# Performance work log

Measured on AMD Instinct MI355X. Metric: run time of the kernel, lower is better.

The kernel has to match this reference:

```python
import jax, jax.numpy as jnp
import numpy as np

NHEAD = 8
ATT_EPS = 1e-6
LN_EPS = 1e-5


def _layernorm(x, g, b):
    mu = jnp.mean(x, axis=-1, keepdims=True)
    var = jnp.mean(jnp.square(x - mu), axis=-1, keepdims=True)
    return (x - mu) * jax.lax.rsqrt(var + LN_EPS) * g + b


def setup_inputs() -> dict:
    key = jax.random.key(0)
    ks = jax.random.split(key, 7)
    N, L, C = 4, 16384, 256
    s = 1.0 / np.sqrt(C)
    return {
        "x": jax.random.normal(ks[0], (N, L, C), jnp.float32),
        "Wq": jax.random.normal(ks[1], (C, C), jnp.float32) * s,
        "Wk": jax.random.normal(ks[2], (C, C), jnp.float32) * s,
        "Wv": jax.random.normal(ks[3], (C, C), jnp.float32) * s,
        "Wm": jax.random.normal(ks[4], (C, C), jnp.float32) * s,
        "W1": jax.random.normal(ks[5], (2 * C, 2 * C), jnp.float32) * (1.0 / np.sqrt(2 * C)),
        "W2": jax.random.normal(ks[6], (2 * C, C), jnp.float32) * (1.0 / np.sqrt(2 * C)),
        "g1": jnp.ones((C,), jnp.float32),
        "b1": jnp.zeros((C,), jnp.float32),
        "g2": jnp.ones((C,), jnp.float32),
        "b2": jnp.zeros((C,), jnp.float32),
    }


def reference(x, Wq, Wk, Wv, Wm, W1, W2, g1, b1, g2, b2):
    N, L, C = x.shape
    H = NHEAD
    D = C // H
    # projections -> [N, L, H, D]
    q = (x @ Wq).reshape(N, L, H, D)
    k = (x @ Wk).reshape(N, L, H, D)
    v = (x @ Wv).reshape(N, L, H, D)
    # elu+1 feature map (linear attention)
    Q = jax.nn.elu(q) + 1.0
    K = jax.nn.elu(k) + 1.0
    v = v / L  # values / v_length
    # KV: [N, H, D, Dv]
    KV = jnp.einsum('nshd,nshv->nhdv', K, v)
    # normalizer Z: [N, L, H]
    Z = 1.0 / (jnp.einsum('nlhd,nhd->nlh', Q, K.sum(axis=1)) + ATT_EPS)
    # queried values, rescaled by v_length
    msg = jnp.einsum('nlhd,nhdv,nlh->nlhv', Q, KV, Z) * L  # [N, L, H, Dv]
    # merge heads + norm1
    msg = msg.reshape(N, L, C) @ Wm
    msg = _layernorm(msg, g1, b1)
    # MLP on concat([x, msg]) + norm2
    h = jnp.concatenate([x, msg], axis=-1) @ W1
    h = jax.nn.relu(h) @ W2
    msg = _layernorm(h, g2, b2)
    return x + msg
```

## Files before the change

kernel.cpp:

```cpp
#include <hip/hip_runtime.h>
#include <hip/hip_bf16.h>
#include <math.h>

#define L_SEQ   16384
#define C_DIM   256
#define N_BATCH 4
#define N_HEAD  8
#define D_H     32
#define M_ROWS  (N_BATCH * L_SEQ)
#define KV_SPLIT 64
#define SLAB_E  ((size_t)M_ROWS * C_DIM)

typedef unsigned short u16;
typedef unsigned int   u32;
typedef short s16x8 __attribute__((ext_vector_type(8)));
typedef float f32x4 __attribute__((ext_vector_type(4)));

__device__ __forceinline__ float bf2f(u32 lo16) { return __uint_as_float(lo16 << 16); }
__device__ __forceinline__ u16 f2bf(float f) {
    u32 u = __float_as_uint(f);
    u32 rb = ((u >> 16) & 1u) + 0x7fffu;
    return (u16)((u + rb) >> 16);
}

__device__ __forceinline__ void gl_lds16(const u16* g, u16* l) {
    __builtin_amdgcn_global_load_lds(
        (__attribute__((address_space(1))) void*)g,
        (__attribute__((address_space(3))) void*)l, 16, 0, 0);
}

__global__ __launch_bounds__(256)
void prep_all(const float* __restrict__ x, u16* __restrict__ xb, int n8,
              const float* __restrict__ Wq, const float* __restrict__ Wk,
              const float* __restrict__ Wv, const float* __restrict__ Wm,
              const float* __restrict__ W1, const float* __restrict__ W2,
              u16* __restrict__ wqkvt, u16* __restrict__ wmt,
              u16* __restrict__ w1t, u16* __restrict__ w2t)
{
    __shared__ float tile[32][33];
    int bt = blockIdx.x;
    if (bt < 2048) {
        int i = bt * 256 + threadIdx.x;
        int stride = 2048 * 256;
        for (; i < n8; i += stride) {
            float4 f0 = ((const float4*)x)[(size_t)i * 2];
            float4 f1 = ((const float4*)x)[(size_t)i * 2 + 1];
            uint4 o;
            o.x = (u32)f2bf(f0.x) | ((u32)f2bf(f0.y) << 16);
            o.y = (u32)f2bf(f0.z) | ((u32)f2bf(f0.w) << 16);
            o.z = (u32)f2bf(f1.x) | ((u32)f2bf(f1.y) << 16);
            o.w = (u32)f2bf(f1.z) | ((u32)f2bf(f1.w) << 16);
            ((uint4*)xb)[i] = o;
        }
        return;
    }
    bt -= 2048;
    const float* src; u16* dst; int K, N, rowoff, tt;
    if (bt < 192)      { int w = bt >> 6; tt = bt & 63;
                         src = (w == 0) ? Wq : (w == 1) ? Wk : Wv;
                         dst = wqkvt; K = 256; N = 256; rowoff = w * 256; }
    else if (bt < 256) { tt = bt - 192; src = Wm; dst = wmt; K = 256; N = 256; rowoff = 0; }
    else if (bt < 512) { tt = bt - 256; src = W1; dst = w1t; K = 512; N = 512; rowoff = 0; }
    else               { tt = bt - 512; src = W2; dst = w2t; K = 512; N = 256; rowoff = 0; }
    int ntx = N >> 5;
    int n0 = (tt % ntx) * 32, k0 = (tt / ntx) * 32;
    int tx = threadIdx.x & 31, ty = threadIdx.x >> 5;
    #pragma unroll
    for (int i = 0; i < 32; i += 8)
        tile[ty + i][tx] = src[(size_t)(k0 + ty + i) * N + n0 + tx];
    __syncthreads();
    #pragma unroll
    for (int i = 0; i < 32; i += 8)
        dst[(size_t)(rowoff + n0 + ty + i) * K + k0 + tx] = f2bf(tile[tx][ty + i]);
}

template<int EPI>
__global__ __launch_bounds__(256)
void gemm128(const u16* __restrict__ A1, const u16* __restrict__ A2,
             int KA, int sA1, int sA2,
             const u16* __restrict__ Bt, int ldb, int bstride,
             u16* __restrict__ C, int ldc, int K, float escale, int nx)
{
    __shared__ __align__(16) u16 smem[16384];

    const int tid = threadIdx.x;
    const int nwg = gridDim.x;
    const int cpx = nwg >> 3;
    const int hb  = blockIdx.x;
    const int lb  = (hb & 7) * cpx + (hb >> 3);
    const int m0 = (lb / nx) * 128;
    const int n0 = (lb % nx) * 128;
    const int w = tid >> 6, lane = tid & 63;
    const int wr = w >> 1, wc = w & 1;
    const int g = lane >> 4, r = lane & 15;

    Bt += (size_t)(m0 / L_SEQ) * bstride;

    const u16 *pA1[2], *pA2[2], *pB[2];
    int loff[2];
    #pragma unroll
    for (int i = 0; i < 2; ++i) {
        int li  = i * 256 + tid;
        int row = li >> 2, kc = li & 3;
        int kcg = kc ^ ((row >> 1) & 3);
        pA1[i] = A1 + (size_t)(m0 + row) * sA1 + kcg * 8;
        pA2[i] = A2 + (size_t)(m0 + row) * sA2 + kcg * 8 - KA;
        pB[i]  = Bt + (size_t)(n0 + row) * ldb + kcg * 8;
        loff[i] = li * 8;
    }

    f32x4 acc[4][4] = {};

    auto stage = [&](int kt, int buf) {
        u16* As_ = smem + buf * 4096;
        u16* Bs_ = smem + 8192 + buf * 4096;
        const int ko = kt * 32;
        #pragma unroll
        for (int i = 0; i < 2; ++i) {
            const u16* Ap = ((ko < KA) ? pA1[i] : pA2[i]) + ko;
            gl_lds16(Ap, &As_[loff[i]]);
            gl_lds16(pB[i] + ko, &Bs_[loff[i]]);
        }
    };

    const int kts = K / 32;
    const int gsw = g ^ ((r >> 1) & 3);
    stage(0, 0);
    for (int kt = 0; kt < kts; ++kt) {
        const int cur = kt & 1;
        asm volatile("s_barrier" ::: "memory");
        if (kt + 1 < kts) {
            stage(kt + 1, cur ^ 1);
            asm volatile("s_waitcnt vmcnt(4)" ::: "memory");
        } else {
            asm volatile("s_waitcnt vmcnt(0)" ::: "memory");
        }
        asm volatile("s_barrier" ::: "memory");

        const u16* Ar = smem + cur * 4096;
        const u16* Br = smem + 8192 + cur * 4096;
        s16x8 a[4], b[4];
        #pragma unroll
        for (int mi = 0; mi < 4; ++mi)
            a[mi] = *(const s16x8*)&Ar[(wr * 64 + mi * 16 + r) * 32 + gsw * 8];
        #pragma unroll
        for (int ni = 0; ni < 4; ++ni)
            b[ni] = *(const s16x8*)&Br[(wc * 64 + ni * 16 + r) * 32 + gsw * 8];
        __builtin_amdgcn_s_setprio(1);
        #pragma unroll
        for (int mi = 0; mi < 4; ++mi)
            #pragma unroll
            for (int ni = 0; ni < 4; ++ni)
                asm volatile("v_mfma_f32_16x16x32_bf16 %0, %1, %2, %0"
                             : "+v"(acc[mi][ni]) : "v"(b[ni]), "v"(a[mi]));
        __builtin_amdgcn_s_setprio(0);
    }

    asm volatile("s_nop 7");
    asm volatile("s_nop 7");

    __syncthreads();
    char* ct = (char*)smem;
    #pragma unroll
    for (int mi = 0; mi < 4; ++mi) {
        int rl = wr * 64 + mi * 16 + r;
        #pragma unroll
        for (int ni = 0; ni < 4; ++ni) {
            int cl = wc * 64 + ni * 16 + g * 4;
            int gc = n0 + cl;
            ushort4 o;
            #pragma unroll
            for (int j = 0; j < 4; ++j) {
                float v = acc[mi][ni][j];
                if (EPI == 3)      v = (v > 0.f) ? v : 0.f;
                else if (EPI == 4) v = (gc < 512) ? ((v > 0.f) ? (v + 1.f) : __expf(v))
                                                  : v * escale;
                (&o.x)[j] = f2bf(v);
            }
            int byte = (rl * 256 + cl * 2) ^ ((rl & 7) << 4);
            *(ushort4*)(ct + byte) = o;
        }
    }
    __syncthreads();
    {
        const int rr = tid >> 4, ck = tid & 15;
        u16* slab = C; int coff = n0;
        if (EPI == 4) {
            slab = (n0 < 256) ? C : (n0 < 512) ? C + SLAB_E : C + 2 * SLAB_E;
            coff = n0 & 255;
        }
        #pragma unroll
        for (int it = 0; it < 8; ++it) {
            int rl = it * 16 + rr;
            int byte = (rl * 256 + ck * 16) ^ ((rl & 7) << 4);
            uint4 val = *(const uint4*)(ct + byte);
            size_t row = (size_t)(m0 + rl);
            if (EPI == 4)
                *(uint4*)(slab + row * 256 + coff + ck * 8) = val;
            else
                *(uint4*)(C + row * (size_t)ldc + coff + ck * 8) = val;
        }
    }
}

template<int EPI>
__global__ __launch_bounds__(256)
void gemm_ln(const u16* __restrict__ A1, const u16* __restrict__ A2,
             int KA, int sA1, int sA2,
             const u16* __restrict__ Bt, int ldb, int bstride,
             u16* __restrict__ C, int ldc, int K, float escale, int nx,
             const float* __restrict__ gw, const float* __restrict__ bw,
             const float* __restrict__ xres, float* __restrict__ outf)
{
    __shared__ __align__(16) u16 smem[24576];
    __shared__ float red[4][2][128];

    const int tid = threadIdx.x;
    const int nwg = gridDim.x;
    const int cpx = nwg >> 3;
    const int hb  = blockIdx.x;
    const int lb  = (hb & 7) * cpx + (hb >> 3);
    const int m0 = (lb / nx) * 128;
    const int n0 = (lb % nx) * 256;
    const int wc = tid >> 6;
    const int lane = tid & 63;
    const int g = lane >> 4, r = lane & 15;

    const u16* Btb = Bt + (size_t)(m0 / L_SEQ) * bstride;

    const u16 *pA1[2], *pA2[2], *pB[4];
    int loffA[2], loffB[4];
    #pragma unroll
    for (int i = 0; i < 2; ++i) {
        int li  = i * 256 + tid;
        int row = li >> 2, kc = li & 3;
        int kcg = kc ^ ((row >> 1) & 3);
        pA1[i] = A1 + (size_t)(m0 + row) * sA1 + kcg * 8;
        pA2[i] = A2 + (size_t)(m0 + row) * sA2 + kcg * 8 - KA;
        loffA[i] = li * 8;
    }
    #pragma unroll
    for (int i = 0; i < 4; ++i) {
        int li  = i * 256 + tid;
        int row = li >> 2, kc = li & 3;
        int kcg = kc ^ ((row >> 1) & 3);
        pB[i] = Btb + (size_t)(n0 + row) * ldb + kcg * 8;
        loffB[i] = li * 8;
    }

    f32x4 acc[8][4] = {};

    auto stage = [&](int kt, int buf) {
        u16* As_ = smem + buf * 4096;
        u16* Bs_ = smem + 8192 + buf * 8192;
        const int ko = kt * 32;
        #pragma unroll
        for (int i = 0; i < 2; ++i) {
            const u16* Ap = ((ko < KA) ? pA1[i] : pA2[i]) + ko;
            gl_lds16(Ap, &As_[loffA[i]]);
        }
        #pragma unroll
        for (int i = 0; i < 4; ++i)
            gl_lds16(pB[i] + ko, &Bs_[loffB[i]]);
    };

    const int kts = K / 32;
    const int gsw = g ^ ((r >> 1) & 3);
    stage(0, 0);
    for (int kt = 0; kt < kts; ++kt) {
        const int cur = kt & 1;
        asm volatile("s_barrier" ::: "memory");
        if (kt + 1 < kts) {
            stage(kt + 1, cur ^ 1);
            asm volatile("s_waitcnt vmcnt(6)" ::: "memory");
        } else {
            asm volatile("s_waitcnt vmcnt(0)" ::: "memory");
        }
        asm volatile("s_barrier" ::: "memory");

        const u16* Ar = smem + cur * 4096;
        const u16* Br = smem + 8192 + cur * 8192;
        s16x8 b[4];
        #pragma unroll
        for (int ni = 0; ni < 4; ++ni)
            b[ni] = *(const s16x8*)&Br[(wc * 64 + ni * 16 + r) * 32 + gsw * 8];
        __builtin_amdgcn_s_setprio(1);
        #pragma unroll
        for (int mi = 0; mi < 8; ++mi) {
            s16x8 av = *(const s16x8*)&Ar[(mi * 16 + r) * 32 + gsw * 8];
            #pragma unroll
            for (int ni = 0; ni < 4; ++ni)
                asm volatile("v_mfma_f32_16x16x32_bf16 %0, %1, %2, %0"
                             : "+v"(acc[mi][ni]) : "v"(b[ni]), "v"(av));
        }
        __builtin_amdgcn_s_setprio(0);
    }

    asm volatile("s_nop 7");
    asm volatile("s_nop 7");

    #pragma unroll
    for (int mi = 0; mi < 8; ++mi) {
        float s = 0.f, s2 = 0.f;
        #pragma unroll
        for (int ni = 0; ni < 4; ++ni)
            #pragma unroll
            for (int j = 0; j < 4; ++j) {
                float v = acc[mi][ni][j];
                s += v; s2 += v * v;
            }
        s  += __shfl_xor(s, 16);  s  += __shfl_xor(s, 32);
        s2 += __shfl_xor(s2, 16); s2 += __shfl_xor(s2, 32);
        if (g == 0) {
            red[wc][0][mi * 16 + r] = s;
            red[wc][1][mi * 16 + r] = s2;
        }
    }
    __syncthreads();

    float4 gv[4], bv[4];
    #pragma unroll
    for (int ni = 0; ni < 4; ++ni) {
        int c = wc * 64 + ni * 16 + g * 4;
        gv[ni] = *(const float4*)&gw[c];
        bv[ni] = *(const float4*)&bw[c];
    }

    char* ct = (char*)smem;
    if (EPI == 5) {
        #pragma unroll
        for (int h = 0; h < 2; ++h) {
            __syncthreads();
            #pragma unroll
            for (int mi2 = 0; mi2 < 4; ++mi2) {
                int mi = h * 4 + mi2;
                int rlg = mi * 16 + r;
                int rl = rlg - h * 64;
                float S  = red[0][0][rlg] + red[1][0][rlg] + red[2][0][rlg] + red[3][0][rlg];
                float S2 = red[0][1][rlg] + red[1][1][rlg] + red[2][1][rlg] + red[3][1][rlg];
                float mu = S * (1.0f / 256.0f);
                float var = S2 * (1.0f / 256.0f) - mu * mu;
                float rstd = rsqrtf(var + 1e-5f);
                #pragma unroll
                for (int ni = 0; ni < 4; ++ni) {
                    int cl = wc * 64 + ni * 16 + g * 4;
                    ushort4 o;
                    o.x = f2bf((acc[mi][ni][0] - mu) * rstd * gv[ni].x + bv[ni].x);
                    o.y = f2bf((acc[mi][ni][1] - mu) * rstd * gv[ni].y + bv[ni].y);
                    o.z = f2bf((acc[mi][ni][2] - mu) * rstd * gv[ni].z + bv[ni].z);
                    o.w = f2bf((acc[mi][ni][3] - mu) * rstd * gv[ni].w + bv[ni].w);
                    int byte = (rl * 512 + cl * 2) ^ ((rl & 7) << 4);
                    *(ushort4*)(ct + byte) = o;
                }
            }
            __syncthreads();
            const int rr = tid >> 5, ck = tid & 31;
            #pragma unroll
            for (int it = 0; it < 8; ++it) {
                int rl = it * 8 + rr;
                int byte = (rl * 512 + ck * 16) ^ ((rl & 7) << 4);
                uint4 val = *(const uint4*)(ct + byte);
                size_t row = (size_t)(m0 + h * 64 + rl);
                *(uint4*)(C + row * 256 + ck * 8) = val;
            }
        }
    } else {
        #pragma unroll
        for (int qd = 0; qd < 4; ++qd) {
            __syncthreads();
            #pragma unroll
            for (int mi2 = 0; mi2 < 2; ++mi2) {
                int mi = qd * 2 + mi2;
                int rlg = mi * 16 + r;
                int rl = rlg - qd * 32;
                float S  = red[0][0][rlg] + red[1][0][rlg] + red[2][0][rlg] + red[3][0][rlg];
                float S2 = red[0][1][rlg] + red[1][1][rlg] + red[2][1][rlg] + red[3][1][rlg];
                float mu = S * (1.0f / 256.0f);
                float var = S2 * (1.0f / 256.0f) - mu * mu;
                float rstd = rsqrtf(var + 1e-5f);
                #pragma unroll
                for (int ni = 0; ni < 4; ++ni) {
                    int cl = wc * 64 + ni * 16 + g * 4;
                    float4 o;
                    o.x = (acc[mi][ni][0] - mu) * rstd * gv[ni].x + bv[ni].x;
                    o.y = (acc[mi][ni][1] - mu) * rstd * gv[ni].y + bv[ni].y;
                    o.z = (acc[mi][ni][2] - mu) * rstd * gv[ni].z + bv[ni].z;
                    o.w = (acc[mi][ni][3] - mu) * rstd * gv[ni].w + bv[ni].w;
                    int byte = (rl * 1024 + cl * 4) ^ ((rl & 7) << 4);
                    *(float4*)(ct + byte) = o;
                }
            }
            __syncthreads();
            const int rr = tid >> 6, ck = tid & 63;
            #pragma unroll
            for (int it = 0; it < 8; ++it) {
                int rl = it * 4 + rr;
                int byte = (rl * 1024 + ck * 16) ^ ((rl & 7) << 4);
                float4 val = *(const float4*)(ct + byte);
                size_t row = (size_t)(m0 + qd * 32 + rl);
                float4 xv = *(const float4*)&xres[row * 256 + ck * 4];
                val.x += xv.x; val.y += xv.y; val.z += xv.z; val.w += xv.w;
                *(float4*)&outf[row * 256 + ck * 4] = val;
            }
        }
    }
}

__global__ __launch_bounds__(256)
void kv_partial(const u16* __restrict__ Kf, const u16* __restrict__ Vf, int ld,
                float* __restrict__ part)
{
    int b  = blockIdx.x;
    int s  = b & (KV_SPLIT - 1);
    int nh = b / KV_SPLIT;
    int h  = nh & (N_HEAD - 1);
    int n  = nh / N_HEAD;
    int t  = threadIdx.x;

    __shared__ __align__(16) float Ks[32][D_H];
    __shared__ __align__(16) float Vs[32][D_H];

    const int d   = t >> 3;
    const int dv0 = (t & 7) * 4;
    const int lr  = t >> 3;
    const int lc  = (t & 7) * 4;
    const size_t base = ((size_t)n * L_SEQ) * ld + h * D_H;

    float a0 = 0, a1 = 0, a2 = 0, a3 = 0, asum = 0;
    const int CH = L_SEQ / KV_SPLIT;
    for (int l = s * CH; l < s * CH + CH; l += 32) {
        __syncthreads();
        uint2 ku = *(const uint2*)&Kf[base + (size_t)(l + lr) * ld + lc];
        uint2 vu = *(const uint2*)&Vf[base + (size_t)(l + lr) * ld + lc];
        Ks[lr][lc] = bf2f(ku.x & 0xffff); Ks[lr][lc + 1] = bf2f(ku.x >> 16);
        Ks[lr][lc + 2] = bf2f(ku.y & 0xffff); Ks[lr][lc + 3] = bf2f(ku.y >> 16);
        Vs[lr][lc] = bf2f(vu.x & 0xffff); Vs[lr][lc + 1] = bf2f(vu.x >> 16);
        Vs[lr][lc + 2] = bf2f(vu.y & 0xffff); Vs[lr][lc + 3] = bf2f(vu.y >> 16);
        __syncthreads();
        #pragma unroll
        for (int i = 0; i < 32; ++i) {
            float kv = Ks[i][d];
            float4 vv = *(const float4*)&Vs[i][dv0];
            a0 = fmaf(kv, vv.x, a0);
            a1 = fmaf(kv, vv.y, a1);
            a2 = fmaf(kv, vv.z, a2);
            a3 = fmaf(kv, vv.w, a3);
            asum += kv;
        }
    }
    float* p = part + (size_t)b * 1056;
    p[d * D_H + dv0 + 0] = a0;
    p[d * D_H + dv0 + 1] = a1;
    p[d * D_H + dv0 + 2] = a2;
    p[d * D_H + dv0 + 3] = a3;
    if ((t & 7) == 0) p[1024 + d] = asum;
}

__global__ __launch_bounds__(256)
void kv_final(const float* __restrict__ part, float* __restrict__ Ksum,
              u16* __restrict__ bdr)
{
    __shared__ float KVs[D_H][D_H];
    int nh = blockIdx.x;
    int h  = nh & (N_HEAD - 1);
    int n  = nh / N_HEAD;
    int t  = threadIdx.x;

    float ax = 0, ay = 0, az = 0, aw = 0, ssum = 0;
    const float* p0 = part + (size_t)nh * KV_SPLIT * 1056;
    for (int s = 0; s < KV_SPLIT; ++s) {
        const float* p = p0 + (size_t)s * 1056;
        float4 v = *(const float4*)&p[t * 4];
        ax += v.x; ay += v.y; az += v.z; aw += v.w;
        if (t < D_H) ssum += p[1024 + t];
    }
    const int d = t >> 3, dv0 = (t & 7) * 4;
    KVs[d][dv0] = ax; KVs[d][dv0 + 1] = ay; KVs[d][dv0 + 2] = az; KVs[d][dv0 + 3] = aw;
    if (t < D_H) Ksum[nh * D_H + t] = ssum;
    __syncthreads();

    const int rr = t >> 3;
    const int c0 = (t & 7) * 32;
    u16* dst = bdr + ((size_t)n * 256 + h * 32 + rr) * 256 + c0;
    if (c0 == h * 32) {
        #pragma unroll
        for (int j = 0; j < 32; j += 4) {
            float4 vv = *(const float4*)&KVs[rr][j];
            ushort4 o;
            o.x = f2bf(vv.x); o.y = f2bf(vv.y); o.z = f2bf(vv.z); o.w = f2bf(vv.w);
            *(ushort4*)(dst + j) = o;
        }
    } else {
        uint4 z = make_uint4(0, 0, 0, 0);
        #pragma unroll
        for (int j = 0; j < 32; j += 8)
            *(uint4*)(dst + j) = z;
    }
}

#define NT_TOK 32
__global__ __launch_bounds__(256)
void attn_z(u16* __restrict__ q, const float* __restrict__ Ksum)
{
    const int t = threadIdx.x;
    const int w = t >> 6, lane = t & 63;
    const int tok0 = blockIdx.x * NT_TOK;
    const int n = tok0 / L_SEQ;
    float4 ks = *(const float4*)&Ksum[n * C_DIM + lane * 4];

    for (int i = 0; i < NT_TOK; i += 4) {
        int tok = tok0 + i + w;
        u16* qp = q + (size_t)tok * C_DIM + lane * 4;
        uint2 qu = *(const uint2*)qp;
        float q0 = bf2f(qu.x & 0xffff), q1 = bf2f(qu.x >> 16);
        float q2 = bf2f(qu.y & 0xffff), q3 = bf2f(qu.y >> 16);
        float p = q0 * ks.x + q1 * ks.y + q2 * ks.z + q3 * ks.w;
        p += __shfl_xor(p, 1);
        p += __shfl_xor(p, 2);
        p += __shfl_xor(p, 4);
        float z = (float)L_SEQ / (p + 1e-6f);
        uint2 o;
        o.x = (u32)f2bf(q0 * z) | ((u32)f2bf(q1 * z) << 16);
        o.y = (u32)f2bf(q2 * z) | ((u32)f2bf(q3 * z) << 16);
        *(uint2*)qp = o;
    }
}

extern "C" void kernel_launch(void* const* d_in, const int* in_sizes, int n_in,
                              void* d_out, int out_size, void* d_ws, size_t ws_size,
                              hipStream_t stream)
{
    const float* x  = (const float*)d_in[0];
    const float* Wq = (const float*)d_in[1];
    const float* Wk = (const float*)d_in[2];
    const float* Wv = (const float*)d_in[3];
    const float* Wm = (const float*)d_in[4];
    const float* W1 = (const float*)d_in[5];
    const float* W2 = (const float*)d_in[6];
    const float* g1 = (const float*)d_in[7];
    const float* b1 = (const float*)d_in[8];
    const float* g2 = (const float*)d_in[9];
    const float* b2 = (const float*)d_in[10];
    float* out = (float*)d_out;

    u16* xb  = (u16*)d_ws;
    u16* q   = xb + SLAB_E;
    u16* k   = q + SLAB_E;
    u16* v   = k + SLAB_E;
    u16* ln1 = v + SLAB_E;
    u16* h   = q;
    u16* wqkvt = ln1 + SLAB_E;
    u16* wmt   = wqkvt + 768 * 256;
    u16* w1t   = wmt + 256 * 256;
    u16* w2t   = w1t + 512 * 512;
    u16* bdr   = w2t + 256 * 512;
    u16* bdwt  = bdr + (size_t)N_BATCH * 256 * 256;
    float* Ksum = (float*)(bdwt + (size_t)N_BATCH * 256 * 256);
    float* part = Ksum + (size_t)N_BATCH * N_HEAD * D_H;

    dim3 blk(256);
    const float invL = 1.0f / (float)L_SEQ;

    prep_all<<<2688, blk, 0, stream>>>(x, xb, (int)(SLAB_E / 8),
                                       Wq, Wk, Wv, Wm, W1, W2,
                                       wqkvt, wmt, w1t, w2t);

    gemm128<4><<<(M_ROWS / 128) * 6, blk, 0, stream>>>(
        xb, xb, 256, 256, 256, wqkvt, 256, 0, q, 256, 256, invL, 6);

    kv_partial<<<N_BATCH * N_HEAD * KV_SPLIT, blk, 0, stream>>>(k, v, 256, part);
    kv_final<<<N_BATCH * N_HEAD, blk, 0, stream>>>(part, Ksum, bdr);

    gemm128<0><<<16, blk, 0, stream>>>(
        wmt, wmt, 256, 256, 256, bdr, 256, 0, bdwt, 1024, 256, 1.f, 8);

    attn_z<<<M_ROWS / NT_TOK, blk, 0, stream>>>(q, Ksum);

    gemm_ln<5><<<M_ROWS / 128, blk, 0, stream>>>(
        q, q, 256, 256, 256, bdwt, 1024, 256, ln1, 256, 256, 1.f, 1,
        g1, b1, nullptr, nullptr);

    gemm128<3><<<(M_ROWS / 128) * 4, blk, 0, stream>>>(
        xb, ln1, 256, 256, 256, w1t, 512, 0, h, 512, 512, 1.f, 4);

    gemm_ln<6><<<M_ROWS / 128, blk, 0, stream>>>(
        h, h, 512, 512, 512, w2t, 512, 0, nullptr, 256, 512, 1.f, 1,
        g2, b2, x, out);
}
```

Measured before the change: 231.9 us.

## Add 128x256 wide-tile GEMM for QKV projection and MLP first layer

Adds a gemm_wide kernel in which each workgroup computes a 128x256 output tile, with each of the four waves owning a 64-column strip across all 128 rows. It replaces the 128x128 gemm128 for the QKV projection and the W1 MLP GEMM. Each workgroup loads the A tile once for twice the output width, which roughly halves A-operand global traffic and launches half as many workgroups. The costs are a larger register accumulator (8x4 tiles per wave), more shared memory, fewer blocks for occupancy, and an epilogue split into two halves; gemm128 keeps only the plain bf16 epilogue.

```diff
diff --git a/kernel.cpp b/kernel.cpp
--- a/kernel.cpp
+++ b/kernel.cpp
@@ -76,6 +76,141 @@
 
 template<int EPI>
 __global__ __launch_bounds__(256)
+void gemm_wide(const u16* __restrict__ A1, const u16* __restrict__ A2,
+               int KA, int sA1, int sA2,
+               const u16* __restrict__ Bt, int ldb,
+               u16* __restrict__ C, int ldc, int K, float escale, int nx)
+{
+    __shared__ __align__(16) u16 smem[24576];
+
+    const int tid = threadIdx.x;
+    const int nwg = gridDim.x;
+    const int cpx = nwg >> 3;
+    const int hb  = blockIdx.x;
+    const int lb  = (hb & 7) * cpx + (hb >> 3);
+    const int m0 = (lb / nx) * 128;
+    const int n0 = (lb % nx) * 256;
+    const int wcv = tid >> 6;
+    const int lane = tid & 63;
+    const int g = lane >> 4, r = lane & 15;
+
+    const u16 *pA1[2], *pA2[2], *pB[4];
+    int loffA[2], loffB[4];
+    #pragma unroll
+    for (int i = 0; i < 2; ++i) {
+        int li  = i * 256 + tid;
+        int row = li >> 2, kc = li & 3;
+        int kcg = kc ^ ((row >> 1) & 3);
+        pA1[i] = A1 + (size_t)(m0 + row) * sA1 + kcg * 8;
+        pA2[i] = A2 + (size_t)(m0 + row) * sA2 + kcg * 8 - KA;
+        loffA[i] = li * 8;
+    }
+    #pragma unroll
+    for (int i = 0; i < 4; ++i) {
+        int li  = i * 256 + tid;
+        int row = li >> 2, kc = li & 3;
+        int kcg = kc ^ ((row >> 1) & 3);
+        pB[i] = Bt + (size_t)(n0 + row) * ldb + kcg * 8;
+        loffB[i] = li * 8;
+    }
+
+    f32x4 acc[8][4] = {};
+
+    auto stage = [&](int kt, int buf) {
+        u16* As_ = smem + buf * 4096;
+        u16* Bs_ = smem + 8192 + buf * 8192;
+        const int ko = kt * 32;
+        #pragma unroll
+        for (int i = 0; i < 2; ++i) {
+            const u16* Ap = ((ko < KA) ? pA1[i] : pA2[i]) + ko;
+            gl_lds16(Ap, &As_[loffA[i]]);
+        }
+        #pragma unroll
+        for (int i = 0; i < 4; ++i)
+            gl_lds16(pB[i] + ko, &Bs_[loffB[i]]);
+    };
+
+    const int kts = K / 32;
+    const int gsw = g ^ ((r >> 1) & 3);
+    stage(0, 0);
+    for (int kt = 0; kt < kts; ++kt) {
+        const int cur = kt & 1;
+        asm volatile("s_barrier" ::: "memory");
+        if (kt + 1 < kts) {
+            stage(kt + 1, cur ^ 1);
+            asm volatile("s_waitcnt vmcnt(6)" ::: "memory");
+        } else {
+            asm volatile("s_waitcnt vmcnt(0)" ::: "memory");
+        }
+        asm volatile("s_barrier" ::: "memory");
+
+        const u16* Ar = smem + cur * 4096;
+        const u16* Br = smem + 8192 + cur * 8192;
+        s16x8 b[4];
+        #pragma unroll
+        for (int ni = 0; ni < 4; ++ni)
+            b[ni] = *(const s16x8*)&Br[(wcv * 64 + ni * 16 + r) * 32 + gsw * 8];
+        __builtin_amdgcn_s_setprio(1);
+        #pragma unroll
+        for (int mi = 0; mi < 8; ++mi) {
+            s16x8 av = *(const s16x8*)&Ar[(mi * 16 + r) * 32 + gsw * 8];
+            #pragma unroll
+            for (int ni = 0; ni < 4; ++ni)
+                asm volatile("v_mfma_f32_16x16x32_bf16 %0, %1, %2, %0"
+                             : "+v"(acc[mi][ni]) : "v"(b[ni]), "v"(av));
+        }
+        __builtin_amdgcn_s_setprio(0);
+    }
+
+    asm volatile("s_nop 7");
+    asm volatile("s_nop 7");
+
+    const bool vslab = (EPI == 4) && (n0 >= 512);
+    u16* outp;
+    if (EPI == 4) outp = C + (size_t)(n0 >> 8) * SLAB_E;
+    else          outp = C + n0;
+    char* ct = (char*)smem;
+    #pragma unroll
+    for (int hh = 0; hh < 2; ++hh) {
+        __syncthreads();
+        #pragma unroll
+        for (int mi2 = 0; mi2 < 4; ++mi2) {
+            int mi = hh * 4 + mi2;
+            int rl = mi2 * 16 + r;
+            #pragma unroll
+            for (int ni = 0; ni < 4; ++ni) {
+                int cl = wcv * 64 + ni * 16 + g * 4;
+                ushort4 o;
+                #pragma unroll
+                for (int j = 0; j < 4; ++j) {
+                    float v = acc[mi][ni][j];
+                    if (EPI == 3)      v = (v > 0.f) ? v : 0.f;
+                    else if (EPI == 4) v = vslab ? v * escale
+                                                 : ((v > 0.f) ? (v + 1.f) : __expf(v));
+                    (&o.x)[j] = f2bf(v);
+                }
+                int byte = (rl * 512 + cl * 2) ^ ((rl & 7) << 4);
+                *(ushort4*)(ct + byte) = o;
+            }
+        }
+        __syncthreads();
+        const int rr = tid >> 5, ck = tid & 31;
+        #pragma unroll
+        for (int it = 0; it < 8; ++it) {
+            int rl = it * 8 + rr;
+            int byte = (rl * 512 + ck * 16) ^ ((rl & 7) << 4);
+            uint4 val = *(const uint4*)(ct + byte);
+            size_t row = (size_t)(m0 + hh * 64 + rl);
+            if (EPI == 4)
+                *(uint4*)(outp + row * 256 + ck * 8) = val;
+            else
+                *(uint4*)(outp + row * (size_t)ldc + ck * 8) = val;
+        }
+    }
+}
+
+template<int EPI>
+__global__ __launch_bounds__(256)
 void gemm128(const u16* __restrict__ A1, const u16* __restrict__ A2,
              int KA, int sA1, int sA2,
              const u16* __restrict__ Bt, int ldb, int bstride,
@@ -167,16 +302,10 @@
         #pragma unroll
         for (int ni = 0; ni < 4; ++ni) {
             int cl = wc * 64 + ni * 16 + g * 4;
-            int gc = n0 + cl;
             ushort4 o;
             #pragma unroll
-            for (int j = 0; j < 4; ++j) {
-                float v = acc[mi][ni][j];
-                if (EPI == 3)      v = (v > 0.f) ? v : 0.f;
-                else if (EPI == 4) v = (gc < 512) ? ((v > 0.f) ? (v + 1.f) : __expf(v))
-                                                  : v * escale;
-                (&o.x)[j] = f2bf(v);
-            }
+            for (int j = 0; j < 4; ++j)
+                (&o.x)[j] = f2bf(acc[mi][ni][j]);
             int byte = (rl * 256 + cl * 2) ^ ((rl & 7) << 4);
             *(ushort4*)(ct + byte) = o;
         }
@@ -184,21 +313,13 @@
     __syncthreads();
     {
         const int rr = tid >> 4, ck = tid & 15;
-        u16* slab = C; int coff = n0;
-        if (EPI == 4) {
-            slab = (n0 < 256) ? C : (n0 < 512) ? C + SLAB_E : C + 2 * SLAB_E;
-            coff = n0 & 255;
-        }
         #pragma unroll
         for (int it = 0; it < 8; ++it) {
             int rl = it * 16 + rr;
             int byte = (rl * 256 + ck * 16) ^ ((rl & 7) << 4);
             uint4 val = *(const uint4*)(ct + byte);
             size_t row = (size_t)(m0 + rl);
-            if (EPI == 4)
-                *(uint4*)(slab + row * 256 + coff + ck * 8) = val;
-            else
-                *(uint4*)(C + row * (size_t)ldc + coff + ck * 8) = val;
+            *(uint4*)(C + row * (size_t)ldc + n0 + ck * 8) = val;
         }
     }
 }
@@ -565,8 +686,8 @@
                                        Wq, Wk, Wv, Wm, W1, W2,
                                        wqkvt, wmt, w1t, w2t);
 
-    gemm128<4><<<(M_ROWS / 128) * 6, blk, 0, stream>>>(
-        xb, xb, 256, 256, 256, wqkvt, 256, 0, q, 256, 256, invL, 6);
+    gemm_wide<4><<<(M_ROWS / 128) * 3, blk, 0, stream>>>(
+        xb, xb, 256, 256, 256, wqkvt, 256, q, 256, 256, invL, 3);
 
     kv_partial<<<N_BATCH * N_HEAD * KV_SPLIT, blk, 0, stream>>>(k, v, 256, part);
     kv_final<<<N_BATCH * N_HEAD, blk, 0, stream>>>(part, Ksum, bdr);
@@ -580,8 +701,8 @@
         q, q, 256, 256, 256, bdwt, 1024, 256, ln1, 256, 256, 1.f, 1,
         g1, b1, nullptr, nullptr);
 
-    gemm128<3><<<(M_ROWS / 128) * 4, blk, 0, stream>>>(
-        xb, ln1, 256, 256, 256, w1t, 512, 0, h, 512, 512, 1.f, 4);
+    gemm_wide<3><<<(M_ROWS / 128) * 2, blk, 0, stream>>>(
+        xb, ln1, 256, 256, 256, w1t, 512, h, 512, 512, 1.f, 2);
 
     gemm_ln<6><<<M_ROWS / 128, blk, 0, stream>>>(
         h, h, 512, 512, 512, w2t, 512, 0, nullptr, 256, 512, 1.f, 1,
```

After: 238.9 us. 3.0% more time.
